# Optimization experiments

Measured on AMD Instinct MI355X. Metric: run time of the kernel, lower is better.

## Reference

```python
import jax, jax.numpy as jnp
import numpy as np

B, T, HID = 4, 2048, 2048
N_HEAD, N_KV, HD = 16, 2, 128
N_REP = N_HEAD // N_KV


def setup_inputs() -> dict:
    key = jax.random.key(0)
    ks = jax.random.split(key, 7)
    s = 0.02
    return {
        "x": jax.random.normal(ks[0], (B, T, HID), jnp.float32),
        "cos": jax.random.normal(ks[1], (T, 1, HD // 2), jnp.float32),
        "sin": jax.random.normal(ks[2], (T, 1, HD // 2), jnp.float32),
        "Wq": jax.random.normal(ks[3], (N_HEAD * HD, HID), jnp.float32) * s,
        "Wk": jax.random.normal(ks[4], (N_KV * HD, HID), jnp.float32) * s,
        "Wv": jax.random.normal(ks[5], (N_KV * HD, HID), jnp.float32) * s,
        "Wo": jax.random.normal(ks[6], (HID, HID), jnp.float32) * s,
    }


def _rope(x, cos, sin):
    # x: (B, T, H, HD); cos/sin: (T, 1, HD//2) broadcast over B and H
    x_r = x[..., 0::2]
    x_i = x[..., 1::2]
    out_r = x_r * cos - x_i * sin
    out_i = x_r * sin + x_i * cos
    return jnp.stack([out_r, out_i], axis=-1).reshape(x.shape)


def _rms_norm(x):
    eps = jnp.finfo(x.dtype).eps
    var = jnp.mean(jnp.square(x), axis=-1, keepdims=True)
    return x * jax.lax.rsqrt(var + eps)


def reference(x, cos, sin, Wq, Wk, Wv, Wo):
    b, t, _ = x.shape
    q = (x @ Wq.T).reshape(b, t, N_HEAD, HD)
    k = (x @ Wk.T).reshape(b, t, N_KV, HD)
    v = (x @ Wv.T).reshape(b, t, N_KV, HD)
    q = _rms_norm(_rope(q, cos, sin))
    k = _rms_norm(_rope(k, cos, sin))
    # GQA without materializing repeated K/V: group q heads per kv head
    # q: (b, t, n_kv, n_rep, hd) -> (b, n_kv, n_rep, t, hd)
    q = q.reshape(b, t, N_KV, N_REP, HD).transpose(0, 2, 3, 1, 4)
    k = k.transpose(0, 2, 1, 3)  # (b, n_kv, t, hd)
    v = v.transpose(0, 2, 1, 3)
    scale = 1.0 / jnp.sqrt(jnp.asarray(HD, x.dtype))
    scores = jnp.einsum("bgrtd,bgsd->bgrts", q, k) * scale
    causal = jnp.tril(jnp.ones((t, t), dtype=bool))
    scores = jnp.where(causal, scores, jnp.asarray(-jnp.inf, scores.dtype))
    attn = jax.nn.softmax(scores, axis=-1)
    y = jnp.einsum("bgrts,bgsd->bgrtd", attn, v)
    # (b, n_kv, n_rep, t, hd) -> (b, t, n_head*hd)
    y = y.transpose(0, 3, 1, 2, 4).reshape(b, t, N_HEAD * HD)
    return y @ Wo.T
```

## Files before the change

kernel.cpp:

```cpp
#include <hip/hip_runtime.h>

#define B_    4
#define T_    2048
#define HID_  2048
#define NH_   16
#define NKV_  2
#define HD_   128
#define M_    (B_ * T_)
#define NQKV_ 2560

typedef __bf16 bf16x8 __attribute__((ext_vector_type(8)));
typedef float  f32x4  __attribute__((ext_vector_type(4)));

#define AS1 __attribute__((address_space(1)))
#define AS3 __attribute__((address_space(3)))

#if __has_builtin(__builtin_amdgcn_exp2f)
#define EXP2(x) __builtin_amdgcn_exp2f(x)
#else
#define EXP2(x) exp2f(x)
#endif

__device__ __forceinline__ void load_lds16(const void* g, void* l) {
  __builtin_amdgcn_global_load_lds((const AS1 unsigned int*)g,
                                   (AS3 unsigned int*)l, 16, 0, 0);
}

__device__ __forceinline__ unsigned short f2bf(float x) {
  union { float f; unsigned u; } a; a.f = x;
  unsigned r = a.u + 0x7fffu + ((a.u >> 16) & 1u);
  return (unsigned short)(r >> 16);
}
__device__ __forceinline__ float bf2f(unsigned h) {
  union { unsigned u; float f; } a; a.u = h << 16;
  return a.f;
}
__device__ __forceinline__ unsigned pk_rtz(float lo, float hi) {
  union { float f; unsigned u; } a, b; a.f = lo; b.f = hi;
  return (a.u >> 16) | (b.u & 0xffff0000u);
}

__global__ __launch_bounds__(256) void cast_bf16(const float* __restrict__ in,
                                                 unsigned short* __restrict__ out,
                                                 int n4) {
  int i = blockIdx.x * 256 + threadIdx.x;
  if (i >= n4) return;
  float4 v = ((const float4*)in)[i];
  ushort4 o;
  o.x = f2bf(v.x); o.y = f2bf(v.y); o.z = f2bf(v.z); o.w = f2bf(v.w);
  ((ushort4*)out)[i] = o;
}

template <int OUT_BF16>
__global__ __launch_bounds__(256) void gemm_bt(const unsigned short* __restrict__ A,
                                               const unsigned short* __restrict__ Bm,
                                               void* __restrict__ C,
                                               int M, int N, int K) {
  __shared__ __align__(16) unsigned short As[128 * 32];
  __shared__ __align__(16) unsigned short Bs[128 * 32];
  const int tid = threadIdx.x;
  const int w = tid >> 6, lane = tid & 63;
  const int m0 = blockIdx.y << 7, n0 = blockIdx.x << 7;
  const int c = lane & 15, grp = lane >> 4;
  const int lr = lane >> 2, lc = (lane & 3) << 3;
  const int wm = (w & 1) << 6, wn = (w >> 1) << 6;
  f32x4 acc[4][4] = {};
  for (int k0 = 0; k0 < K; k0 += 32) {
    __syncthreads();
    {
      int r0 = w << 4;
      load_lds16(A + (size_t)(m0 + r0 + lr) * K + k0 + lc, &As[r0 * 32]);
      load_lds16(A + (size_t)(m0 + 64 + r0 + lr) * K + k0 + lc, &As[(64 + r0) * 32]);
      load_lds16(Bm + (size_t)(n0 + r0 + lr) * K + k0 + lc, &Bs[r0 * 32]);
      load_lds16(Bm + (size_t)(n0 + 64 + r0 + lr) * K + k0 + lc, &Bs[(64 + r0) * 32]);
    }
    __syncthreads();
    bf16x8 af[4], bf[4];
#pragma unroll
    for (int i = 0; i < 4; i++)
      af[i] = *(const bf16x8*)&As[(wm + i * 16 + c) * 32 + grp * 8];
#pragma unroll
    for (int j = 0; j < 4; j++)
      bf[j] = *(const bf16x8*)&Bs[(wn + j * 16 + c) * 32 + grp * 8];
#pragma unroll
    for (int i = 0; i < 4; i++)
#pragma unroll
      for (int j = 0; j < 4; j++)
        acc[i][j] = __builtin_amdgcn_mfma_f32_16x16x32_bf16(af[i], bf[j], acc[i][j], 0, 0, 0);
  }
#pragma unroll
  for (int i = 0; i < 4; i++)
#pragma unroll
    for (int j = 0; j < 4; j++)
#pragma unroll
      for (int r = 0; r < 4; r++) {
        int row = m0 + wm + i * 16 + grp * 4 + r;
        int col = n0 + wn + j * 16 + c;
        float v = acc[i][j][r];
        if (OUT_BF16) ((unsigned short*)C)[(size_t)row * N + col] = f2bf(v);
        else          ((float*)C)[(size_t)row * N + col] = v;
      }
}

__global__ __launch_bounds__(256) void rope_norm(const unsigned short* __restrict__ qkv,
                                                 const float* __restrict__ cosb,
                                                 const float* __restrict__ sinb,
                                                 unsigned short* __restrict__ qo,
                                                 unsigned short* __restrict__ ko,
                                                 unsigned short* __restrict__ vo) {
  const int m = blockIdx.x;
  const int b = m >> 11, t = m & 2047;
  const int w = threadIdx.x >> 6, lane = threadIdx.x & 63;
  const float cv = cosb[t * 64 + lane], sv = sinb[t * 64 + lane];
  const unsigned short* row = qkv + (size_t)m * NQKV_;
  const float QSCL = 0.08838834764831845f * 1.4426950408889634f;
  for (int hh = w; hh < 20; hh += 4) {
    if (hh < 18) {
      const int col0 = (hh < 16) ? hh * 128 : 2048 + (hh - 16) * 128;
      unsigned pr = *(const unsigned*)(row + col0 + 2 * lane);
      float xr = bf2f(pr & 0xffffu), xi = bf2f(pr >> 16);
      float orr = xr * cv - xi * sv;
      float oi  = xr * sv + xi * cv;
      float ss = orr * orr + oi * oi;
#pragma unroll
      for (int off = 1; off < 64; off <<= 1) ss += __shfl_xor(ss, off);
      float scl = rsqrtf(ss * (1.0f / 128.0f) + 1.1920929e-07f);
      if (hh < 16) {
        float s2 = scl * QSCL;
        unsigned out = (unsigned)f2bf(orr * s2) | ((unsigned)f2bf(oi * s2) << 16);
        *(unsigned*)(qo + (((size_t)(b * NH_ + hh)) * T_ + t) * HD_ + 2 * lane) = out;
      } else {
        unsigned out = (unsigned)f2bf(orr * scl) | ((unsigned)f2bf(oi * scl) << 16);
        *(unsigned*)(ko + (((size_t)(b * NKV_ + (hh - 16))) * T_ + t) * HD_ + 2 * lane) = out;
      }
    } else {
      const int gg = hh - 18;
      unsigned pr = *(const unsigned*)(row + 2304 + gg * 128 + 2 * lane);
      *(unsigned*)(vo + (((size_t)(b * NKV_ + gg)) * T_ + t) * HD_ + 2 * lane) = pr;
    }
  }
}

__global__ __launch_bounds__(256) void transpose_v(const unsigned short* __restrict__ v,
                                                   unsigned short* __restrict__ vt) {
  __shared__ unsigned short tile[64][65];
  const int bg = blockIdx.z;
  const int t0 = blockIdx.x << 6, h0 = blockIdx.y << 6;
  const unsigned short* src = v + (size_t)bg * T_ * HD_;
  unsigned short* dst = vt + (size_t)bg * T_ * HD_;
  const int tid = threadIdx.x;
  const int rr = tid >> 4, cc = (tid & 15) << 2;
#pragma unroll
  for (int it = 0; it < 4; it++) {
    int r = rr + it * 16;
    ushort4 d = *(const ushort4*)(src + (size_t)(t0 + r) * HD_ + h0 + cc);
    tile[r][cc + 0] = d.x; tile[r][cc + 1] = d.y;
    tile[r][cc + 2] = d.z; tile[r][cc + 3] = d.w;
  }
  __syncthreads();
#pragma unroll
  for (int it = 0; it < 4; it++) {
    int r = rr + it * 16;
    ushort4 d;
    d.x = tile[cc + 0][r]; d.y = tile[cc + 1][r];
    d.z = tile[cc + 2][r]; d.w = tile[cc + 3][r];
    *(ushort4*)(dst + (size_t)(h0 + r) * T_ + t0 + cc) = d;
  }
}

__global__ __launch_bounds__(256, 2) void flash_attn(const unsigned short* __restrict__ q,
                                                     const unsigned short* __restrict__ k,
                                                     const unsigned short* __restrict__ vt,
                                                     unsigned short* __restrict__ y) {
  __shared__ __align__(16) unsigned short Kb[4 * 128 * 32];
  __shared__ __align__(16) unsigned short Vb[4 * 128 * 32];
  const int tid = threadIdx.x;
  const int w = tid >> 6, lane = tid & 63;
  const int c = lane & 15, grp = lane >> 4;
  const int lr = lane >> 2, lc = (lane & 3) << 3;
  const int t0 = (15 - (int)blockIdx.x) << 7;
  const int hq = blockIdx.y, b = blockIdx.z, g = hq >> 3;
  const unsigned short* qbase = q + (((size_t)(b * NH_ + hq)) * T_ + t0) * HD_;
  const unsigned short* kbase = k + ((size_t)(b * NKV_ + g)) * T_ * HD_;
  const unsigned short* vtbase = vt + ((size_t)(b * NKV_ + g)) * HD_ * T_;

  bf16x8 qf[2][4];
#pragma unroll
  for (int ti = 0; ti < 2; ti++)
#pragma unroll
    for (int ks = 0; ks < 4; ks++)
      qf[ti][ks] = *(const bf16x8*)(qbase + (size_t)(w * 32 + ti * 16 + c) * HD_ + ks * 32 + grp * 8);

  f32x4 oacc[2][8] = {};
  float mrun[2], lrun[2];
  mrun[0] = mrun[1] = -__builtin_inff();
  lrun[0] = lrun[1] = 0.f;

  const int swl = (((lane & 3) << 1) ^ (lr & 6)) << 2;
  const int sw = c & 6;

  for (int s0 = 0; s0 <= t0; s0 += 128) {
    __syncthreads();
#pragma unroll
    for (int kc = 0; kc < 4; kc++) {
#pragma unroll
      for (int jj = 0; jj < 2; jj++) {
        int rb = w * 32 + jj * 16;
        load_lds16(kbase + (size_t)(s0 + rb + lr) * HD_ + kc * 32 + lc, &Kb[kc * 4096 + rb * 32]);
        load_lds16(vtbase + (size_t)(rb + lr) * T_ + s0 + kc * 32 + swl, &Vb[kc * 4096 + rb * 32]);
      }
    }
    __syncthreads();

    f32x4 st[2][8] = {};
#pragma unroll
    for (int ks = 0; ks < 4; ks++) {
#pragma unroll
      for (int kvt = 0; kvt < 8; kvt++) {
        bf16x8 ak = *(const bf16x8*)&Kb[ks * 4096 + (kvt * 16 + c) * 32 + grp * 8];
        st[0][kvt] = __builtin_amdgcn_mfma_f32_16x16x32_bf16(ak, qf[0][ks], st[0][kvt], 0, 0, 0);
        st[1][kvt] = __builtin_amdgcn_mfma_f32_16x16x32_bf16(ak, qf[1][ks], st[1][kvt], 0, 0, 0);
      }
    }
    if (s0 == t0) {
#pragma unroll
      for (int ti = 0; ti < 2; ti++)
#pragma unroll
        for (int kvt = 0; kvt < 8; kvt++)
#pragma unroll
          for (int r = 0; r < 4; r++) {
            int kv = kvt * 16 + grp * 4 + r;
            int qq = w * 32 + ti * 16 + c;
            if (kv > qq) st[ti][kvt][r] = -__builtin_inff();
          }
    }

    unsigned pkv[2][8][2];
#pragma unroll
    for (int ti = 0; ti < 2; ti++) {
      float rm = st[ti][0][0];
#pragma unroll
      for (int kvt = 0; kvt < 8; kvt++)
#pragma unroll
        for (int r = 0; r < 4; r++) rm = fmaxf(rm, st[ti][kvt][r]);
      rm = fmaxf(rm, __shfl_xor(rm, 16));
      rm = fmaxf(rm, __shfl_xor(rm, 32));
      float mnew = fmaxf(mrun[ti], rm);
      float alpha = EXP2(mrun[ti] - mnew);
      mrun[ti] = mnew;
      float rs = 0.f;
#pragma unroll
      for (int kvt = 0; kvt < 8; kvt++) {
        float p0 = EXP2(st[ti][kvt][0] - mnew);
        float p1 = EXP2(st[ti][kvt][1] - mnew);
        float p2 = EXP2(st[ti][kvt][2] - mnew);
        float p3 = EXP2(st[ti][kvt][3] - mnew);
        rs += (p0 + p1) + (p2 + p3);
        pkv[ti][kvt][0] = pk_rtz(p0, p1);
        pkv[ti][kvt][1] = pk_rtz(p2, p3);
      }
      rs += __shfl_xor(rs, 16);
      rs += __shfl_xor(rs, 32);
      lrun[ti] = lrun[ti] * alpha + rs;
#pragma unroll
      for (int hj = 0; hj < 8; hj++)
#pragma unroll
        for (int r = 0; r < 4; r++) oacc[ti][hj][r] *= alpha;
    }

#pragma unroll
    for (int ks = 0; ks < 4; ks++) {
      union { int4 i; bf16x8 v; } pf0, pf1;
      pf0.i = make_int4(pkv[0][2 * ks][0], pkv[0][2 * ks][1], pkv[0][2 * ks + 1][0], pkv[0][2 * ks + 1][1]);
      pf1.i = make_int4(pkv[1][2 * ks][0], pkv[1][2 * ks][1], pkv[1][2 * ks + 1][0], pkv[1][2 * ks + 1][1]);
#pragma unroll
      for (int hj = 0; hj < 8; hj++) {
        const unsigned short* vrow = &Vb[ks * 4096 + (hj * 16 + c) * 32];
        int u0 = (grp ^ sw) << 2;
        uint2 v0 = *(const uint2*)(vrow + u0);
        uint2 v1 = *(const uint2*)(vrow + (u0 ^ 16));
        union { int4 i; bf16x8 v; } av;
        av.i = make_int4((int)v0.x, (int)v0.y, (int)v1.x, (int)v1.y);
        oacc[0][hj] = __builtin_amdgcn_mfma_f32_16x16x32_bf16(av.v, pf0.v, oacc[0][hj], 0, 0, 0);
        oacc[1][hj] = __builtin_amdgcn_mfma_f32_16x16x32_bf16(av.v, pf1.v, oacc[1][hj], 0, 0, 0);
      }
    }
  }

#pragma unroll
  for (int ti = 0; ti < 2; ti++) {
    float inv = 1.f / lrun[ti];
    int trow = t0 + w * 32 + ti * 16 + c;
#pragma unroll
    for (int hj = 0; hj < 8; hj++) {
      ushort4 o;
      o.x = f2bf(oacc[ti][hj][0] * inv);
      o.y = f2bf(oacc[ti][hj][1] * inv);
      o.z = f2bf(oacc[ti][hj][2] * inv);
      o.w = f2bf(oacc[ti][hj][3] * inv);
      *(ushort4*)&y[((size_t)(b * T_ + trow)) * HID_ + hq * HD_ + hj * 16 + grp * 4] = o;
    }
  }
}

extern "C" void kernel_launch(void* const* d_in, const int* in_sizes, int n_in,
                              void* d_out, int out_size, void* d_ws, size_t ws_size,
                              hipStream_t stream) {
  const float* x    = (const float*)d_in[0];
  const float* cosb = (const float*)d_in[1];
  const float* sinb = (const float*)d_in[2];
  const float* Wq   = (const float*)d_in[3];
  const float* Wk   = (const float*)d_in[4];
  const float* Wv   = (const float*)d_in[5];
  const float* Wo   = (const float*)d_in[6];
  float* out = (float*)d_out;

  char* ws = (char*)d_ws;
  size_t off = 0;
  auto take = [&](size_t elems) {
    unsigned short* p = (unsigned short*)(ws + off);
    off += ((elems * 2 + 255) & ~(size_t)255);
    return p;
  };
  unsigned short* xb   = take((size_t)M_ * HID_);
  unsigned short* wqkv = take((size_t)NQKV_ * HID_);
  unsigned short* wob  = take((size_t)HID_ * HID_);
  unsigned short* qkv  = take((size_t)M_ * NQKV_);
  unsigned short* qb   = take((size_t)B_ * NH_ * T_ * HD_);
  unsigned short* kb   = take((size_t)B_ * NKV_ * T_ * HD_);
  unsigned short* vb   = take((size_t)B_ * NKV_ * T_ * HD_);
  unsigned short* vtb  = take((size_t)B_ * NKV_ * T_ * HD_);
  unsigned short* yb   = take((size_t)M_ * HID_);
  (void)ws_size; (void)in_sizes; (void)n_in; (void)out_size;

  cast_bf16<<<16384, 256, 0, stream>>>(x, xb, 4194304);
  cast_bf16<<<4096, 256, 0, stream>>>(Wq, wqkv, 1048576);
  cast_bf16<<<512, 256, 0, stream>>>(Wk, wqkv + (size_t)2048 * 2048, 131072);
  cast_bf16<<<512, 256, 0, stream>>>(Wv, wqkv + (size_t)2304 * 2048, 131072);
  cast_bf16<<<4096, 256, 0, stream>>>(Wo, wob, 1048576);

  gemm_bt<1><<<dim3(20, 64), 256, 0, stream>>>(xb, wqkv, qkv, M_, NQKV_, HID_);
  rope_norm<<<8192, 256, 0, stream>>>(qkv, cosb, sinb, qb, kb, vb);
  transpose_v<<<dim3(32, 2, 8), 256, 0, stream>>>(vb, vtb);
  flash_attn<<<dim3(16, 16, 4), 256, 0, stream>>>(qb, kb, vtb, yb);
  gemm_bt<0><<<dim3(16, 64), 256, 0, stream>>>(yb, wob, out, M_, HID_, HID_);
}
```

Measured before the change: 553.1 us.

## Double-buffer flash attention KV tiles, swizzle GEMM LDS, fuse weight casts

Flash attention now walks the keys in 64-wide chunks through double-buffered LDS, prefetching the next chunk while the current one is computed. Each wave masks at its own 32-row granularity and skips chunks that lie wholly above its causal diagonal. The GEMM and attention LDS layouts gain an XOR swizzle to avoid bank conflicts, the V transpose read order is permuted, and the three Q/K/V weight casts are merged into one launch. The smaller chunks mean more loop iterations and barriers, and the double buffers use more LDS, which can limit occupancy.

```diff
diff --git a/kernel.cpp b/kernel.cpp
--- a/kernel.cpp
+++ b/kernel.cpp
@@ -46,6 +46,21 @@
   int i = blockIdx.x * 256 + threadIdx.x;
   if (i >= n4) return;
   float4 v = ((const float4*)in)[i];
+  ushort4 o;
+  o.x = f2bf(v.x); o.y = f2bf(v.y); o.z = f2bf(v.z); o.w = f2bf(v.w);
+  ((ushort4*)out)[i] = o;
+}
+
+__global__ __launch_bounds__(256) void cast_w(const float* __restrict__ Wq,
+                                              const float* __restrict__ Wk,
+                                              const float* __restrict__ Wv,
+                                              unsigned short* __restrict__ out) {
+  int i = blockIdx.x * 256 + threadIdx.x;
+  const float* src; int j;
+  if (i < 1048576)      { src = Wq; j = i; }
+  else if (i < 1179648) { src = Wk; j = i - 1048576; }
+  else                  { src = Wv; j = i - 1179648; }
+  float4 v = ((const float4*)src)[j];
   ushort4 o;
   o.x = f2bf(v.x); o.y = f2bf(v.y); o.z = f2bf(v.z); o.w = f2bf(v.w);
   ((ushort4*)out)[i] = o;
@@ -62,26 +77,28 @@
   const int w = tid >> 6, lane = tid & 63;
   const int m0 = blockIdx.y << 7, n0 = blockIdx.x << 7;
   const int c = lane & 15, grp = lane >> 4;
-  const int lr = lane >> 2, lc = (lane & 3) << 3;
+  const int lr = lane >> 2;
+  const int su = (((lane & 3) ^ ((lr >> 1) & 3)) << 3);
+  const int sw = (c >> 1) & 3;
   const int wm = (w & 1) << 6, wn = (w >> 1) << 6;
   f32x4 acc[4][4] = {};
   for (int k0 = 0; k0 < K; k0 += 32) {
     __syncthreads();
     {
       int r0 = w << 4;
-      load_lds16(A + (size_t)(m0 + r0 + lr) * K + k0 + lc, &As[r0 * 32]);
-      load_lds16(A + (size_t)(m0 + 64 + r0 + lr) * K + k0 + lc, &As[(64 + r0) * 32]);
-      load_lds16(Bm + (size_t)(n0 + r0 + lr) * K + k0 + lc, &Bs[r0 * 32]);
-      load_lds16(Bm + (size_t)(n0 + 64 + r0 + lr) * K + k0 + lc, &Bs[(64 + r0) * 32]);
+      load_lds16(A + (size_t)(m0 + r0 + lr) * K + k0 + su, &As[r0 * 32]);
+      load_lds16(A + (size_t)(m0 + 64 + r0 + lr) * K + k0 + su, &As[(64 + r0) * 32]);
+      load_lds16(Bm + (size_t)(n0 + r0 + lr) * K + k0 + su, &Bs[r0 * 32]);
+      load_lds16(Bm + (size_t)(n0 + 64 + r0 + lr) * K + k0 + su, &Bs[(64 + r0) * 32]);
     }
     __syncthreads();
     bf16x8 af[4], bf[4];
 #pragma unroll
     for (int i = 0; i < 4; i++)
-      af[i] = *(const bf16x8*)&As[(wm + i * 16 + c) * 32 + grp * 8];
+      af[i] = *(const bf16x8*)&As[(wm + i * 16 + c) * 32 + ((grp ^ sw) << 3)];
 #pragma unroll
     for (int j = 0; j < 4; j++)
-      bf[j] = *(const bf16x8*)&Bs[(wn + j * 16 + c) * 32 + grp * 8];
+      bf[j] = *(const bf16x8*)&Bs[(wn + j * 16 + c) * 32 + ((grp ^ sw) << 3)];
 #pragma unroll
     for (int i = 0; i < 4; i++)
 #pragma unroll
@@ -150,6 +167,8 @@
   unsigned short* dst = vt + (size_t)bg * T_ * HD_;
   const int tid = threadIdx.x;
   const int rr = tid >> 4, cc = (tid & 15) << 2;
+  const int u = (cc >> 2) & 7;
+  const int cp = (cc & 32) + 16 * (u & 1) + 4 * ((u >> 1) & 3);
 #pragma unroll
   for (int it = 0; it < 4; it++) {
     int r = rr + it * 16;
@@ -162,8 +181,8 @@
   for (int it = 0; it < 4; it++) {
     int r = rr + it * 16;
     ushort4 d;
-    d.x = tile[cc + 0][r]; d.y = tile[cc + 1][r];
-    d.z = tile[cc + 2][r]; d.w = tile[cc + 3][r];
+    d.x = tile[cp + 0][r]; d.y = tile[cp + 1][r];
+    d.z = tile[cp + 2][r]; d.w = tile[cp + 3][r];
     *(ushort4*)(dst + (size_t)(h0 + r) * T_ + t0 + cc) = d;
   }
 }
@@ -172,13 +191,16 @@
                                                      const unsigned short* __restrict__ k,
                                                      const unsigned short* __restrict__ vt,
                                                      unsigned short* __restrict__ y) {
-  __shared__ __align__(16) unsigned short Kb[4 * 128 * 32];
-  __shared__ __align__(16) unsigned short Vb[4 * 128 * 32];
+  __shared__ __align__(16) unsigned short Kb[2][8192];
+  __shared__ __align__(16) unsigned short Vb[2][8192];
   const int tid = threadIdx.x;
   const int w = tid >> 6, lane = tid & 63;
   const int c = lane & 15, grp = lane >> 4;
-  const int lr = lane >> 2, lc = (lane & 3) << 3;
+  const int lr = lane >> 2;
+  const int sw = (c >> 1) & 3;
+  const int su = (((lane & 3) ^ ((lr >> 1) & 3)) << 3);
   const int t0 = (15 - (int)blockIdx.x) << 7;
+  const int t0w = t0 + w * 32;
   const int hq = blockIdx.y, b = blockIdx.z, g = hq >> 3;
   const unsigned short* qbase = q + (((size_t)(b * NH_ + hq)) * T_ + t0) * HD_;
   const unsigned short* kbase = k + ((size_t)(b * NKV_ + g)) * T_ * HD_;
@@ -196,95 +218,97 @@
   mrun[0] = mrun[1] = -__builtin_inff();
   lrun[0] = lrun[1] = 0.f;
 
-  const int swl = (((lane & 3) << 1) ^ (lr & 6)) << 2;
-  const int sw = c & 6;
-
-  for (int s0 = 0; s0 <= t0; s0 += 128) {
-    __syncthreads();
-#pragma unroll
-    for (int kc = 0; kc < 4; kc++) {
-#pragma unroll
-      for (int jj = 0; jj < 2; jj++) {
-        int rb = w * 32 + jj * 16;
-        load_lds16(kbase + (size_t)(s0 + rb + lr) * HD_ + kc * 32 + lc, &Kb[kc * 4096 + rb * 32]);
-        load_lds16(vtbase + (size_t)(rb + lr) * T_ + s0 + kc * 32 + swl, &Vb[kc * 4096 + rb * 32]);
+  auto stage = [&](int s0, int bb) {
+    const unsigned short* kp = kbase + (size_t)(s0 + w * 16 + lr) * HD_ + su;
+#pragma unroll
+    for (int dc = 0; dc < 4; dc++)
+      load_lds16(kp + dc * 32, &Kb[bb][dc * 2048 + (w * 16) * 32]);
+    const unsigned short* vp = vtbase + s0 + su;
+#pragma unroll
+    for (int ks = 0; ks < 2; ks++)
+#pragma unroll
+      for (int jj = 0; jj < 2; jj++)
+        load_lds16(vp + (size_t)(w * 32 + jj * 16 + lr) * T_ + ks * 32,
+                   &Vb[bb][ks * 4096 + (w * 32 + jj * 16) * 32]);
+  };
+
+  const int nch = (t0 >> 6) + 2;
+  stage(0, 0);
+  __syncthreads();
+  for (int ic = 0; ic < nch; ic++) {
+    const int s0 = ic << 6, bb = ic & 1;
+    if (ic + 1 < nch) stage((ic + 1) << 6, bb ^ 1);
+    if (s0 <= t0w + 31) {
+      const unsigned short* Kc = Kb[bb];
+      const unsigned short* Vc = Vb[bb];
+      f32x4 st[2][4] = {};
+#pragma unroll
+      for (int s = 0; s < 4; s++)
+#pragma unroll
+        for (int kvt = 0; kvt < 4; kvt++) {
+          bf16x8 ak = *(const bf16x8*)&Kc[s * 2048 + (kvt * 16 + c) * 32 + ((grp ^ sw) << 3)];
+          st[0][kvt] = __builtin_amdgcn_mfma_f32_16x16x32_bf16(ak, qf[0][s], st[0][kvt], 0, 0, 0);
+          st[1][kvt] = __builtin_amdgcn_mfma_f32_16x16x32_bf16(ak, qf[1][s], st[1][kvt], 0, 0, 0);
+        }
+      if (s0 + 63 > t0w) {
+#pragma unroll
+        for (int ti = 0; ti < 2; ti++)
+#pragma unroll
+          for (int kvt = 0; kvt < 4; kvt++)
+#pragma unroll
+            for (int r = 0; r < 4; r++) {
+              int kv = s0 + kvt * 16 + grp * 4 + r;
+              int qq = t0w + ti * 16 + c;
+              if (kv > qq) st[ti][kvt][r] = -__builtin_inff();
+            }
+      }
+      unsigned pkv[2][4][2];
+#pragma unroll
+      for (int ti = 0; ti < 2; ti++) {
+        float rm = st[ti][0][0];
+#pragma unroll
+        for (int kvt = 0; kvt < 4; kvt++)
+#pragma unroll
+          for (int r = 0; r < 4; r++) rm = fmaxf(rm, st[ti][kvt][r]);
+        rm = fmaxf(rm, __shfl_xor(rm, 16));
+        rm = fmaxf(rm, __shfl_xor(rm, 32));
+        float mnew = fmaxf(mrun[ti], rm);
+        float alpha = EXP2(mrun[ti] - mnew);
+        mrun[ti] = mnew;
+        float rs = 0.f;
+#pragma unroll
+        for (int kvt = 0; kvt < 4; kvt++) {
+          float p0 = EXP2(st[ti][kvt][0] - mnew);
+          float p1 = EXP2(st[ti][kvt][1] - mnew);
+          float p2 = EXP2(st[ti][kvt][2] - mnew);
+          float p3 = EXP2(st[ti][kvt][3] - mnew);
+          rs += (p0 + p1) + (p2 + p3);
+          pkv[ti][kvt][0] = pk_rtz(p0, p1);
+          pkv[ti][kvt][1] = pk_rtz(p2, p3);
+        }
+        rs += __shfl_xor(rs, 16);
+        rs += __shfl_xor(rs, 32);
+        lrun[ti] = lrun[ti] * alpha + rs;
+#pragma unroll
+        for (int hj = 0; hj < 8; hj++)
+#pragma unroll
+          for (int r = 0; r < 4; r++) oacc[ti][hj][r] *= alpha;
+      }
+#pragma unroll
+      for (int s = 0; s < 2; s++) {
+        union { int4 i; bf16x8 v; } pf0, pf1;
+        pf0.i = make_int4(pkv[0][2 * s][0], pkv[0][2 * s][1], pkv[0][2 * s + 1][0], pkv[0][2 * s + 1][1]);
+        pf1.i = make_int4(pkv[1][2 * s][0], pkv[1][2 * s][1], pkv[1][2 * s + 1][0], pkv[1][2 * s + 1][1]);
+#pragma unroll
+        for (int hj = 0; hj < 8; hj++) {
+          union { int4 i; bf16x8 v; } av;
+          av.i = *(const int4*)&Vc[s * 4096 + (hj * 16 + c) * 32 + ((grp ^ sw) << 3)];
+          oacc[0][hj] = __builtin_amdgcn_mfma_f32_16x16x32_bf16(av.v, pf0.v, oacc[0][hj], 0, 0, 0);
+          oacc[1][hj] = __builtin_amdgcn_mfma_f32_16x16x32_bf16(av.v, pf1.v, oacc[1][hj], 0, 0, 0);
+        }
       }
     }
     __syncthreads();
-
-    f32x4 st[2][8] = {};
-#pragma unroll
-    for (int ks = 0; ks < 4; ks++) {
-#pragma unroll
-      for (int kvt = 0; kvt < 8; kvt++) {
-        bf16x8 ak = *(const bf16x8*)&Kb[ks * 4096 + (kvt * 16 + c) * 32 + grp * 8];
-        st[0][kvt] = __builtin_amdgcn_mfma_f32_16x16x32_bf16(ak, qf[0][ks], st[0][kvt], 0, 0, 0);
-        st[1][kvt] = __builtin_amdgcn_mfma_f32_16x16x32_bf16(ak, qf[1][ks], st[1][kvt], 0, 0, 0);
-      }
-    }
-    if (s0 == t0) {
-#pragma unroll
-      for (int ti = 0; ti < 2; ti++)
-#pragma unroll
-        for (int kvt = 0; kvt < 8; kvt++)
-#pragma unroll
-          for (int r = 0; r < 4; r++) {
-            int kv = kvt * 16 + grp * 4 + r;
-            int qq = w * 32 + ti * 16 + c;
-            if (kv > qq) st[ti][kvt][r] = -__builtin_inff();
-          }
-    }
-
-    unsigned pkv[2][8][2];
-#pragma unroll
-    for (int ti = 0; ti < 2; ti++) {
-      float rm = st[ti][0][0];
-#pragma unroll
-      for (int kvt = 0; kvt < 8; kvt++)
-#pragma unroll
-        for (int r = 0; r < 4; r++) rm = fmaxf(rm, st[ti][kvt][r]);
-      rm = fmaxf(rm, __shfl_xor(rm, 16));
-      rm = fmaxf(rm, __shfl_xor(rm, 32));
-      float mnew = fmaxf(mrun[ti], rm);
-      float alpha = EXP2(mrun[ti] - mnew);
-      mrun[ti] = mnew;
-      float rs = 0.f;
-#pragma unroll
-      for (int kvt = 0; kvt < 8; kvt++) {
-        float p0 = EXP2(st[ti][kvt][0] - mnew);
-        float p1 = EXP2(st[ti][kvt][1] - mnew);
-        float p2 = EXP2(st[ti][kvt][2] - mnew);
-        float p3 = EXP2(st[ti][kvt][3] - mnew);
-        rs += (p0 + p1) + (p2 + p3);
-        pkv[ti][kvt][0] = pk_rtz(p0, p1);
-        pkv[ti][kvt][1] = pk_rtz(p2, p3);
-      }
-      rs += __shfl_xor(rs, 16);
-      rs += __shfl_xor(rs, 32);
-      lrun[ti] = lrun[ti] * alpha + rs;
-#pragma unroll
-      for (int hj = 0; hj < 8; hj++)
-#pragma unroll
-        for (int r = 0; r < 4; r++) oacc[ti][hj][r] *= alpha;
-    }
-
-#pragma unroll
-    for (int ks = 0; ks < 4; ks++) {
-      union { int4 i; bf16x8 v; } pf0, pf1;
-      pf0.i = make_int4(pkv[0][2 * ks][0], pkv[0][2 * ks][1], pkv[0][2 * ks + 1][0], pkv[0][2 * ks + 1][1]);
-      pf1.i = make_int4(pkv[1][2 * ks][0], pkv[1][2 * ks][1], pkv[1][2 * ks + 1][0], pkv[1][2 * ks + 1][1]);
-#pragma unroll
-      for (int hj = 0; hj < 8; hj++) {
-        const unsigned short* vrow = &Vb[ks * 4096 + (hj * 16 + c) * 32];
-        int u0 = (grp ^ sw) << 2;
-        uint2 v0 = *(const uint2*)(vrow + u0);
-        uint2 v1 = *(const uint2*)(vrow + (u0 ^ 16));
-        union { int4 i; bf16x8 v; } av;
-        av.i = make_int4((int)v0.x, (int)v0.y, (int)v1.x, (int)v1.y);
-        oacc[0][hj] = __builtin_amdgcn_mfma_f32_16x16x32_bf16(av.v, pf0.v, oacc[0][hj], 0, 0, 0);
-        oacc[1][hj] = __builtin_amdgcn_mfma_f32_16x16x32_bf16(av.v, pf1.v, oacc[1][hj], 0, 0, 0);
-      }
-    }
   }
 
 #pragma unroll
@@ -334,9 +358,7 @@
   (void)ws_size; (void)in_sizes; (void)n_in; (void)out_size;
 
   cast_bf16<<<16384, 256, 0, stream>>>(x, xb, 4194304);
-  cast_bf16<<<4096, 256, 0, stream>>>(Wq, wqkv, 1048576);
-  cast_bf16<<<512, 256, 0, stream>>>(Wk, wqkv + (size_t)2048 * 2048, 131072);
-  cast_bf16<<<512, 256, 0, stream>>>(Wv, wqkv + (size_t)2304 * 2048, 131072);
+  cast_w<<<5120, 256, 0, stream>>>(Wq, Wk, Wv, wqkv);
   cast_bf16<<<4096, 256, 0, stream>>>(Wo, wob, 1048576);
 
   gemm_bt<1><<<dim3(20, 64), 256, 0, stream>>>(xb, wqkv, qkv, M_, NQKV_, HID_);
```

Measured after the change: 549.8 us. About the same (-0.6%).
